# Optimization experiments

Measured on AMD Instinct MI355X. Metric: run time of the kernel, lower is better.

The kernel has to match this reference:

```python
import jax, jax.numpy as jnp
import numpy as np

D = 1024
H = 16
HD = D // H
T = 2048
B = 2
EPS = 1e-6


def rmsnorm(x, w):
    xf = x.astype(jnp.float32)
    n = xf * jax.lax.rsqrt(jnp.mean(xf * xf, axis=-1, keepdims=True) + EPS)
    return n.astype(x.dtype) * w


def setup_inputs() -> dict:
    key = jax.random.key(0)
    ks = jax.random.split(key, 12)
    s_in = 1.0 / np.sqrt(D)
    s_h = 1.0 / np.sqrt(HD * H)
    s_ff = 1.0 / np.sqrt(4 * D)
    return {
        "x": jax.random.normal(ks[0], (B, T, D), jnp.float32),
        "wq": jax.random.normal(ks[1], (H, D, HD), jnp.float32) * s_in,
        "wk": jax.random.normal(ks[2], (H, D, HD), jnp.float32) * s_in,
        "wv": jax.random.normal(ks[3], (H, D, HD), jnp.float32) * s_in,
        "w_proj": jax.random.normal(ks[4], (D, D), jnp.float32) * s_h,
        "b_proj": jax.random.normal(ks[5], (D,), jnp.float32) * 0.01,
        "w1": jax.random.normal(ks[6], (D, 8 * D), jnp.float32) * s_in,
        "b1": jax.random.normal(ks[7], (8 * D,), jnp.float32) * 0.01,
        "w2": jax.random.normal(ks[8], (4 * D, D), jnp.float32) * s_ff,
        "b2": jax.random.normal(ks[9], (D,), jnp.float32) * 0.01,
        "g1": jnp.ones((D,), jnp.float32),
        "g2": jnp.ones((D,), jnp.float32),
    }


def reference(x, wq, wk, wv, w_proj, b_proj, w1, b1, w2, b2, g1, g2):
    # --- attention sub-block ---
    xn = rmsnorm(x, g1)
    q = jnp.einsum("btd,hde->bhte", xn, wq)  # [B,H,T,HD]
    k = jnp.einsum("btd,hde->bhte", xn, wk)
    v = jnp.einsum("btd,hde->bhte", xn, wv)
    scores = jnp.einsum("bhte,bhse->bhts", q, k) * (HD ** -0.5)
    causal = jnp.tril(jnp.ones((T, T), bool))
    scores = jnp.where(causal, scores, -jnp.inf)
    attn = jax.nn.softmax(scores, axis=-1)
    o = jnp.einsum("bhts,bhse->bhte", attn, v)  # [B,H,T,HD]
    o = o.transpose(0, 2, 1, 3).reshape(B, T, H * HD)  # concat heads
    x = x + o @ w_proj + b_proj
    # --- GLU FFN sub-block ---
    xn2 = rmsnorm(x, g2)
    h = xn2 @ w1 + b1  # [B,T,8D]
    a, b = jnp.split(h, 2, axis=-1)
    glu = a * jax.nn.sigmoid(b)  # [B,T,4D]
    x = x + glu @ w2 + b2
    return x
```

## Files before the change

### kernel.cpp

```cpp
#include <hip/hip_runtime.h>


typedef __attribute__((ext_vector_type(4))) float f32x4;
typedef __attribute__((ext_vector_type(8))) short short8;

typedef __attribute__((address_space(1))) const void gvoid;
typedef __attribute__((address_space(3))) void lvoid;

static __device__ __forceinline__ void gl_lds16(const void* g, void* l) {
  __builtin_amdgcn_global_load_lds((gvoid*)g, (lvoid*)l, 16, 0, 0);
}

static __device__ __forceinline__ unsigned short f2bf(float f) {
  union { float f; unsigned u; } v; v.f = f;
  unsigned r = v.u + 0x7fffu + ((v.u >> 16) & 1u);
  return (unsigned short)(r >> 16);
}
static __device__ __forceinline__ float to_f32(float v) { return v; }
static __device__ __forceinline__ float to_f32(unsigned short v) {
  union { unsigned u; float f; } x; x.u = ((unsigned)v) << 16; return x.f;
}

static __device__ __forceinline__ f32x4 mfma16(short8 a, short8 b, f32x4 c) {
  return __builtin_amdgcn_mfma_f32_16x16x32_bf16(a, b, c, 0, 0, 0);
}

template <typename Tin>
__global__ __launch_bounds__(256) void transpose_cvt(
    const Tin* __restrict__ in, unsigned short* __restrict__ out,
    int in_ld, long in_bstride, int out_ld, long out_bstride)
{
  __shared__ float tile[64][65];
  const Tin* inp = in + (long)blockIdx.z * in_bstride;
  unsigned short* outp = out + (long)blockIdx.z * out_bstride;
  int r0 = blockIdx.y * 64, c0 = blockIdx.x * 64;
  int tx = threadIdx.x & 63, ty = threadIdx.x >> 6;
#pragma unroll
  for (int i = ty; i < 64; i += 4)
    tile[i][tx] = to_f32(inp[(long)(r0 + i) * in_ld + (c0 + tx)]);
  __syncthreads();
#pragma unroll
  for (int i = ty; i < 64; i += 4)
    outp[(long)(c0 + i) * out_ld + (r0 + tx)] = f2bf(tile[tx][i]);
}

__global__ __launch_bounds__(256) void qkvw_repack(
    const float* __restrict__ wq, const float* __restrict__ wk,
    const float* __restrict__ wv, unsigned short* __restrict__ out)
{
  __shared__ float tile[64][65];
  const int z = blockIdx.z, head = z & 15, src = z >> 4;
  const float* inp = (src == 0 ? wq : src == 1 ? wk : wv) + (long)head * 1024 * 64;
  unsigned short* outp = out + ((long)src * 1024 + head * 64) * 1024;
  int r0 = blockIdx.y * 64;
  int tx = threadIdx.x & 63, ty = threadIdx.x >> 6;
#pragma unroll
  for (int i = ty; i < 64; i += 4)
    tile[i][tx] = inp[(long)(r0 + i) * 64 + tx];
  __syncthreads();
#pragma unroll
  for (int i = ty; i < 64; i += 4)
    outp[(long)i * 1024 + r0 + tx] = f2bf(tile[tx][i]);
}

__global__ __launch_bounds__(256) void rmsnorm_k(
    const float* __restrict__ x, const float* __restrict__ g,
    unsigned short* __restrict__ out)
{
  int row = blockIdx.x;
  int t = threadIdx.x;
  float4 v = ((const float4*)(x + (long)row * 1024))[t];
  float ss = v.x * v.x + v.y * v.y + v.z * v.z + v.w * v.w;
#pragma unroll
  for (int ofs = 32; ofs; ofs >>= 1) ss += __shfl_down(ss, ofs);
  __shared__ float red[4];
  if ((t & 63) == 0) red[t >> 6] = ss;
  __syncthreads();
  float sc = rsqrtf((red[0] + red[1] + red[2] + red[3]) * (1.0f / 1024.0f) + 1e-6f);
  float4 gv = ((const float4*)g)[t];
  ushort4 o4;
  o4.x = f2bf(v.x * sc * gv.x); o4.y = f2bf(v.y * sc * gv.y);
  o4.z = f2bf(v.z * sc * gv.z); o4.w = f2bf(v.w * sc * gv.w);
  ((ushort4*)(out + (long)row * 1024))[t] = o4;
}

template <int EPI, int BM, int WM_, int WN_, bool GLUB>
__global__ __launch_bounds__(256, 2) void gemm_bt(
    const unsigned short* __restrict__ A, const unsigned short* __restrict__ Bt,
    unsigned short* __restrict__ outb, float* __restrict__ outf,
    const float* __restrict__ res, const float* __restrict__ bias,
    int K, int lda, int ldbt, int ldout)
{
  constexpr int FM = BM / (16 * WM_);
  constexpr int FN = 128 / (16 * WN_);
  constexpr int AR = BM / 32;
  __shared__ alignas(16) unsigned short Asm_[BM * 64];
  __shared__ alignas(16) unsigned short Bsm_[128 * 64];
  const int tid = threadIdx.x, lane = tid & 63, wave = tid >> 6;
  const int lr = lane & 15, lg = lane >> 4;
  const int wr = wave / WN_, wc = wave % WN_;
  const int m0 = blockIdx.y * BM;

  f32x4 acc[FM][FN];
#pragma unroll
  for (int mi = 0; mi < FM; mi++)
#pragma unroll
    for (int ni = 0; ni < FN; ni++) acc[mi][ni] = f32x4{0.f, 0.f, 0.f, 0.f};

  int rr_[4], ru_[4];
  long brow[4];
#pragma unroll
  for (int i = 0; i < 4; i++) {
    int U = tid + 256 * i;
    rr_[i] = U >> 3;
    ru_[i] = ((U & 7) ^ (rr_[i] & 7)) * 8;
    if (GLUB)
      brow[i] = (rr_[i] < 64) ? (long)(blockIdx.x * 64 + rr_[i])
                              : (long)(4096 + blockIdx.x * 64 + rr_[i] - 64);
    else
      brow[i] = (long)blockIdx.x * 128 + rr_[i];
  }

  for (int k0 = 0; k0 < K; k0 += 64) {
#pragma unroll
    for (int i = 0; i < 4; i++) {
      if (i < AR)
        gl_lds16(A + (long)(m0 + rr_[i]) * lda + k0 + ru_[i],
                 (char*)Asm_ + (wave * 64 + 256 * i) * 16);
      gl_lds16(Bt + brow[i] * ldbt + k0 + ru_[i],
               (char*)Bsm_ + (wave * 64 + 256 * i) * 16);
    }
    __syncthreads();

    short8 af[FM][2], bfr[FN][2];
#pragma unroll
    for (int mi = 0; mi < FM; mi++) {
      int row = wr * 16 * FM + mi * 16 + lr;
#pragma unroll
      for (int kk = 0; kk < 2; kk++) {
        int off = row * 128 + (((kk * 4 + lg) ^ (row & 7)) & 7) * 16;
        af[mi][kk] = *(const short8*)((const char*)Asm_ + off);
      }
    }
#pragma unroll
    for (int ni = 0; ni < FN; ni++) {
      int row = wc * 16 * FN + ni * 16 + lr;
#pragma unroll
      for (int kk = 0; kk < 2; kk++) {
        int off = row * 128 + (((kk * 4 + lg) ^ (row & 7)) & 7) * 16;
        bfr[ni][kk] = *(const short8*)((const char*)Bsm_ + off);
      }
    }
#pragma unroll
    for (int kk = 0; kk < 2; kk++)
#pragma unroll
      for (int mi = 0; mi < FM; mi++)
#pragma unroll
        for (int ni = 0; ni < FN; ni++)
          acc[mi][ni] = mfma16(af[mi][kk], bfr[ni][kk], acc[mi][ni]);
    __syncthreads();
  }

  const int rb = m0 + wr * 16 * FM + 4 * lg;
  if constexpr (EPI == 0) {
#pragma unroll
    for (int mi = 0; mi < FM; mi++)
#pragma unroll
      for (int ni = 0; ni < FN; ni++) {
        int col = blockIdx.x * 128 + wc * 16 * FN + ni * 16 + lr;
#pragma unroll
        for (int r = 0; r < 4; r++)
          outb[(long)(rb + mi * 16 + r) * ldout + col] = f2bf(acc[mi][ni][r]);
      }
  } else if constexpr (EPI == 1) {
#pragma unroll
    for (int mi = 0; mi < FM; mi++)
#pragma unroll
      for (int ni = 0; ni < FN; ni++) {
        int col = blockIdx.x * 128 + wc * 16 * FN + ni * 16 + lr;
        float bv = bias[col];
#pragma unroll
        for (int r = 0; r < 4; r++) {
          long idx = (long)(rb + mi * 16 + r) * ldout + col;
          outf[idx] = acc[mi][ni][r] + res[idx] + bv;
        }
      }
  } else {
#pragma unroll
    for (int mi = 0; mi < FM; mi++)
#pragma unroll
      for (int ni = 0; ni < FN / 2; ni++) {
        int col = blockIdx.x * 64 + ni * 16 + lr;
        float ba = bias[col], bb2 = bias[4096 + col];
#pragma unroll
        for (int r = 0; r < 4; r++) {
          float a = acc[mi][ni][r] + ba;
          float b = acc[mi][ni + FN / 2][r] + bb2;
          float s = 1.0f / (1.0f + __expf(-b));
          outb[(long)(rb + mi * 16 + r) * ldout + col] = f2bf(a * s);
        }
      }
  }
}

__global__ __launch_bounds__(256, 2) void attn_k(
    const unsigned short* __restrict__ qkv, const unsigned short* __restrict__ vt,
    unsigned short* __restrict__ o)
{
  __shared__ alignas(16) unsigned short Ksm[2 * 128 * 64];
  __shared__ alignas(16) unsigned short Vsm[2 * 64 * 128];
  __shared__ alignas(16) unsigned short Psm[4][16 * 128];
  const int tid = threadIdx.x, lane = tid & 63, wave = tid >> 6;
  const int lr = lane & 15, lg = lane >> 4;
  const int bh = blockIdx.y, b = bh >> 4, h = bh & 15;
  const int ia = blockIdx.x;
  const int tA0 = ia * 64, tB0 = (31 - ia) * 64;
  const int nchA = (ia + 2) >> 1, nchB = (33 - ia) >> 1;
  const float NEGINF = -__builtin_inff();

  short8 qfA[2], qfB[2];
  {
    const unsigned short* qp =
        qkv + (long)(b * 2048 + tA0 + wave * 16 + lr) * 3072 + h * 64 + lg * 8;
    qfA[0] = *(const short8*)qp;  qfA[1] = *(const short8*)(qp + 32);
    qp = qkv + (long)(b * 2048 + tB0 + wave * 16 + lr) * 3072 + h * 64 + lg * 8;
    qfB[0] = *(const short8*)qp;  qfB[1] = *(const short8*)(qp + 32);
  }
  f32x4 oA[4], oB[4];
#pragma unroll
  for (int n = 0; n < 4; n++) { oA[n] = f32x4{0,0,0,0}; oB[n] = f32x4{0,0,0,0}; }
  float mA = NEGINF, lA = 0.f, mB = NEGINF, lB = 0.f;

  const long kbase = (long)(b * 2048) * 3072 + 1024 + h * 64;
  const long vbase = (long)bh * 64 * 2048;

  auto stage = [&](int buf, int c) {
    const int s0 = c * 128;
#pragma unroll
    for (int i = 0; i < 4; i++) {
      int U = tid + 256 * i;
      int kr = U >> 3, ku = (U ^ kr) & 7;
      gl_lds16(qkv + kbase + (long)(s0 + kr) * 3072 + ku * 8,
               (char*)Ksm + (buf * 1024 + wave * 64 + 256 * i) * 16);
      int vr = U >> 4, vu = (U & 8) | ((U ^ vr) & 7);
      gl_lds16(vt + vbase + (long)vr * 2048 + s0 + vu * 8,
               (char*)Vsm + (buf * 1024 + wave * 64 + 256 * i) * 16);
    }
  };

  char* pb = (char*)&Psm[wave][0];

  auto process = [&](const short8* qf, f32x4* o_acc, float& m, float& l,
                     const char* kb, const char* vb, int s0, int qg, bool diag) {
    f32x4 s[8];
#pragma unroll
    for (int n = 0; n < 8; n++) s[n] = f32x4{0.f, 0.f, 0.f, 0.f};
    __builtin_amdgcn_s_setprio(1);
#pragma unroll
    for (int n = 0; n < 8; n++) {
      int row = n * 16 + lr;
#pragma unroll
      for (int kk = 0; kk < 2; kk++) {
        int off = row * 128 + (((kk * 4 + lg) ^ row) & 7) * 16;
        short8 kf = *(const short8*)(kb + off);
        s[n] = mfma16(kf, qf[kk], s[n]);
      }
    }
    __builtin_amdgcn_s_setprio(0);
#pragma unroll
    for (int n = 0; n < 8; n++)
#pragma unroll
      for (int r = 0; r < 4; r++) {
        float v = s[n][r] * 0.125f;
        if (diag && (s0 + n * 16 + 4 * lg + r > qg)) v = NEGINF;
        s[n][r] = v;
      }
    float t[8];
#pragma unroll
    for (int n = 0; n < 8; n++)
      t[n] = fmaxf(fmaxf(s[n][0], s[n][1]), fmaxf(s[n][2], s[n][3]));
    float mx = fmaxf(fmaxf(fmaxf(t[0], t[1]), fmaxf(t[2], t[3])),
                     fmaxf(fmaxf(t[4], t[5]), fmaxf(t[6], t[7])));
    mx = fmaxf(mx, __shfl_xor(mx, 16));
    mx = fmaxf(mx, __shfl_xor(mx, 32));
    if (!__all(mx <= m + 8.0f)) {
      float mn = fmaxf(m, mx);
      float alpha = __expf(m - mn);
      m = mn;
      l *= alpha;
#pragma unroll
      for (int r = 0; r < 4; r++) {
        float ar = __shfl(alpha, 4 * lg + r);
#pragma unroll
        for (int n = 0; n < 4; n++) o_acc[n][r] *= ar;
      }
    }
    float sum = 0.f;
#pragma unroll
    for (int n = 0; n < 8; n++)
#pragma unroll
      for (int r = 0; r < 4; r++) {
        float p = __expf(s[n][r] - m);
        s[n][r] = p;
        sum += p;
      }
    sum += __shfl_xor(sum, 16);
    sum += __shfl_xor(sum, 32);
    l += sum;
#pragma unroll
    for (int n = 0; n < 8; n++) {
      unsigned lo = (unsigned)f2bf(s[n][0]) | ((unsigned)f2bf(s[n][1]) << 16);
      unsigned hi = (unsigned)f2bf(s[n][2]) | ((unsigned)f2bf(s[n][3]) << 16);
      int u = 2 * n + (lg >> 1);
      int su = (u & 8) | ((u ^ lr) & 7);
      *(uint2*)(pb + lr * 256 + su * 16 + 8 * (lg & 1)) = uint2{lo, hi};
    }
    asm volatile("s_waitcnt lgkmcnt(0)" ::: "memory");
    __builtin_amdgcn_sched_barrier(0);
    short8 pa[4];
#pragma unroll
    for (int ks = 0; ks < 4; ks++) {
      int u = 4 * ks + lg;
      int su = (u & 8) | ((u ^ lr) & 7);
      pa[ks] = *(const short8*)(pb + lr * 256 + su * 16);
    }
    __builtin_amdgcn_s_setprio(1);
#pragma unroll
    for (int n = 0; n < 4; n++) {
      int row = n * 16 + lr;
#pragma unroll
      for (int ks = 0; ks < 4; ks++) {
        int u = 4 * ks + lg;
        int su = (u & 8) | ((u ^ row) & 7);
        short8 vf = *(const short8*)(vb + row * 256 + su * 16);
        o_acc[n] = mfma16(pa[ks], vf, o_acc[n]);
      }
    }
    __builtin_amdgcn_s_setprio(0);
  };

  stage(0, 0);
  __syncthreads();

  const int qgA = tA0 + wave * 16 + lr, qgB = tB0 + wave * 16 + lr;
  for (int c = 0; c < nchB; c++) {
    if (c + 1 < nchB) stage((c + 1) & 1, c + 1);
    const char* kb = (const char*)Ksm + (c & 1) * 16384;
    const char* vb = (const char*)Vsm + (c & 1) * 16384;
    const int s0 = c * 128;
    if (c < nchA) process(qfA, oA, mA, lA, kb, vb, s0, qgA, c == nchA - 1);
    process(qfB, oB, mB, lB, kb, vb, s0, qgB, c == nchB - 1);
    __syncthreads();
  }

  auto finish = [&](const f32x4* o_acc, float l, int t0) {
#pragma unroll
    for (int r = 0; r < 4; r++) {
      float inv = 1.0f / __shfl(l, 4 * lg + r);
      int trow = t0 + wave * 16 + 4 * lg + r;
#pragma unroll
      for (int n = 0; n < 4; n++)
        o[(long)(b * 2048 + trow) * 1024 + h * 64 + n * 16 + lr] =
            f2bf(o_acc[n][r] * inv);
    }
  };
  finish(oA, lA, tA0);
  finish(oB, lB, tB0);
}

extern "C" void kernel_launch(void* const* d_in, const int* in_sizes, int n_in,
                              void* d_out, int out_size, void* d_ws, size_t ws_size,
                              hipStream_t stream) {
  const float* x     = (const float*)d_in[0];
  const float* wq    = (const float*)d_in[1];
  const float* wk    = (const float*)d_in[2];
  const float* wv    = (const float*)d_in[3];
  const float* wproj = (const float*)d_in[4];
  const float* bproj = (const float*)d_in[5];
  const float* w1    = (const float*)d_in[6];
  const float* b1    = (const float*)d_in[7];
  const float* w2    = (const float*)d_in[8];
  const float* b2    = (const float*)d_in[9];
  const float* g1    = (const float*)d_in[10];
  const float* g2    = (const float*)d_in[11];
  (void)in_sizes; (void)n_in; (void)out_size; (void)ws_size;

  char* ws = (char*)d_ws;
  unsigned short* wt_qkv = (unsigned short*)(ws);
  unsigned short* wpt    = (unsigned short*)(ws + (6ul << 20));
  unsigned short* w1t    = (unsigned short*)(ws + (8ul << 20));
  unsigned short* w2t    = (unsigned short*)(ws + (24ul << 20));
  unsigned short* xn     = (unsigned short*)(ws + (32ul << 20));
  unsigned short* qkv    = (unsigned short*)(ws + (40ul << 20));
  unsigned short* vt     = (unsigned short*)(ws + (64ul << 20));
  unsigned short* glu    = (unsigned short*)(ws + (40ul << 20));
  unsigned short* obuf   = (unsigned short*)(ws + (72ul << 20));
  float*          x1     = (float*)(ws + (80ul << 20));
  float* outf = (float*)d_out;

  qkvw_repack<<<dim3(1, 16, 48), 256, 0, stream>>>(wq, wk, wv, wt_qkv);
  transpose_cvt<float><<<dim3(16, 16, 1), 256, 0, stream>>>(
      wproj, wpt, 1024, 0, 1024, 0);
  transpose_cvt<float><<<dim3(128, 16, 1), 256, 0, stream>>>(
      w1, w1t, 8192, 0, 1024, 0);
  transpose_cvt<float><<<dim3(16, 64, 1), 256, 0, stream>>>(
      w2, w2t, 1024, 0, 4096, 0);

  rmsnorm_k<<<4096, 256, 0, stream>>>(x, g1, xn);

  gemm_bt<0, 128, 2, 2, false><<<dim3(24, 32), 256, 0, stream>>>(
      xn, wt_qkv, qkv, nullptr, nullptr, nullptr, 1024, 1024, 1024, 3072);

  transpose_cvt<unsigned short><<<dim3(1, 32, 16), 256, 0, stream>>>(
      qkv + 2048, vt, 3072, 64, 2048, (long)64 * 2048);
  transpose_cvt<unsigned short><<<dim3(1, 32, 16), 256, 0, stream>>>(
      qkv + 2048ul * 3072 + 2048, vt + 16ul * 64 * 2048, 3072, 64, 2048, (long)64 * 2048);

  attn_k<<<dim3(16, 32), 256, 0, stream>>>(qkv, vt, obuf);

  gemm_bt<1, 64, 2, 2, false><<<dim3(8, 64), 256, 0, stream>>>(
      obuf, wpt, nullptr, x1, x, bproj, 1024, 1024, 1024, 1024);

  rmsnorm_k<<<4096, 256, 0, stream>>>(x1, g2, xn);

  gemm_bt<2, 128, 4, 1, true><<<dim3(64, 32), 256, 0, stream>>>(
      xn, w1t, glu, nullptr, nullptr, b1, 1024, 1024, 1024, 4096);

  gemm_bt<1, 64, 2, 2, false><<<dim3(8, 64), 256, 0, stream>>>(
      glu, w2t, nullptr, outf, x1, b2, 4096, 4096, 4096, 1024);
}
```

Baseline: 293.5 us.

## Add 8-wave 256x256-tile GLU GEMM with interleaved load/MFMA pipeline

Replaces the FFN up-projection GEMM with a new 512-thread kernel that computes 256x256 output tiles, with the a and b halves of the GLU interleaved in the B tile so each block emits 128 GLU columns. It double-buffers LDS with direct global-to-LDS loads and interleaves staged loads between MFMA quadrants, separated by barriers and raised wave priority. The goal is more reuse per tile and better overlap of memory with matrix cores. The cost is heavier register and LDS use (64 KB per block), which may limit occupancy.

```diff
diff --git a/kernel.cpp b/kernel.cpp
--- a/kernel.cpp
+++ b/kernel.cpp
@@ -24,6 +24,8 @@
 static __device__ __forceinline__ f32x4 mfma16(short8 a, short8 b, f32x4 c) {
   return __builtin_amdgcn_mfma_f32_16x16x32_bf16(a, b, c, 0, 0, 0);
 }
+
+#define SBAR() asm volatile("s_barrier" ::: "memory")
 
 template <typename Tin>
 __global__ __launch_bounds__(256) void transpose_cvt(
@@ -203,6 +205,164 @@
   }
 }
 
+#define MFMA_Q(AFR, BFR, MI0, NI0)                                          \
+  do {                                                                      \
+    __builtin_amdgcn_s_setprio(1);                                          \
+    _Pragma("unroll") for (int kk_ = 0; kk_ < 2; kk_++)                     \
+    _Pragma("unroll") for (int mi_ = 0; mi_ < 4; mi_++)                     \
+    _Pragma("unroll") for (int ni_ = 0; ni_ < 2; ni_++)                     \
+      acc[(MI0) + mi_][(NI0) + ni_] =                                       \
+          mfma16(AFR[mi_][kk_], BFR[ni_][kk_], acc[(MI0) + mi_][(NI0) + ni_]); \
+    __builtin_amdgcn_s_setprio(0);                                          \
+  } while (0)
+
+__global__ __launch_bounds__(512, 2) void gemm8_glu(
+    const unsigned short* __restrict__ A, const unsigned short* __restrict__ Bt,
+    unsigned short* __restrict__ outb, const float* __restrict__ bias,
+    int K, int lda, int ldbt, int ldout)
+{
+  __shared__ alignas(16) unsigned short Asm_[2][256 * 64];
+  __shared__ alignas(16) unsigned short Bsm_[2][256 * 64];
+  const int tid = threadIdx.x, lane = tid & 63, wave = tid >> 6;
+  const int lr = lane & 15, lg = lane >> 4;
+  const int wr = wave >> 2, wc = wave & 3;
+  const int m0 = blockIdx.y * 256;
+  const int bx = blockIdx.x;
+
+  f32x4 acc[8][4];
+#pragma unroll
+  for (int mi = 0; mi < 8; mi++)
+#pragma unroll
+    for (int ni = 0; ni < 4; ni++) acc[mi][ni] = f32x4{0.f, 0.f, 0.f, 0.f};
+
+  auto stageA = [&](int buf, int h, int k0) {
+#pragma unroll
+    for (int i = 0; i < 2; i++) {
+      int U = tid + 512 * i;
+      int r = U >> 3, s = ((U & 7) ^ (r & 7));
+      gl_lds16(A + (long)(m0 + h * 128 + r) * lda + k0 + s * 8,
+               (char*)&Asm_[buf][0] + h * 16384 + U * 16);
+    }
+  };
+  auto stageB = [&](int buf, int h, int k0) {
+#pragma unroll
+    for (int i = 0; i < 2; i++) {
+      int U = tid + 512 * i;
+      int r = U >> 3, s = ((U & 7) ^ (r & 7));
+      int row = h * 128 + r;
+      int g = row >> 5;
+      long brow = (long)((g & 1) ? 4096 : 0) + bx * 128 + (g >> 1) * 32 + (row & 31);
+      gl_lds16(Bt + brow * ldbt + k0 + s * 8,
+               (char*)&Bsm_[buf][0] + h * 16384 + U * 16);
+    }
+  };
+  auto lda8 = [&](int buf, int mi, int kk) -> short8 {
+    int row = wr * 128 + mi * 16 + lr;
+    return *(const short8*)((const char*)&Asm_[buf][0] + row * 128 +
+                            (((kk * 4 + lg) ^ (row & 7)) * 16));
+  };
+  auto ldb8 = [&](int buf, int ni, int kk) -> short8 {
+    int row = wc * 64 + ni * 16 + lr;
+    return *(const short8*)((const char*)&Bsm_[buf][0] + row * 128 +
+                            (((kk * 4 + lg) ^ (row & 7)) * 16));
+  };
+
+  stageA(0, 0, 0); stageA(0, 1, 0); stageB(0, 0, 0); stageB(0, 1, 0);
+  stageA(1, 0, 64);
+  asm volatile("s_waitcnt vmcnt(2)" ::: "memory");
+  SBAR();
+
+  short8 af[4][2], bf0[2][2], bf1[2][2];
+  const int NIT = K / 128;
+  for (int it = 0; it < NIT; ++it) {
+    const int k0 = it * 128;
+    const bool last = (it == NIT - 1);
+#pragma unroll
+    for (int mi = 0; mi < 4; mi++)
+#pragma unroll
+      for (int kk = 0; kk < 2; kk++) af[mi][kk] = lda8(0, mi, kk);
+#pragma unroll
+    for (int ni = 0; ni < 2; ni++)
+#pragma unroll
+      for (int kk = 0; kk < 2; kk++) bf0[ni][kk] = ldb8(0, ni, kk);
+    stageA(1, 1, k0 + 64);
+    SBAR();
+    MFMA_Q(af, bf0, 0, 0);
+    SBAR();
+#pragma unroll
+    for (int ni = 0; ni < 2; ni++)
+#pragma unroll
+      for (int kk = 0; kk < 2; kk++) bf1[ni][kk] = ldb8(0, ni + 2, kk);
+    stageB(1, 0, k0 + 64);
+    SBAR();
+    MFMA_Q(af, bf1, 0, 2);
+    SBAR();
+#pragma unroll
+    for (int mi = 0; mi < 4; mi++)
+#pragma unroll
+      for (int kk = 0; kk < 2; kk++) af[mi][kk] = lda8(0, mi + 4, kk);
+    stageB(1, 1, k0 + 64);
+    SBAR();
+    MFMA_Q(af, bf1, 4, 2);
+    SBAR();
+    if (!last) stageA(0, 0, k0 + 128);
+    SBAR();
+    MFMA_Q(af, bf0, 4, 0);
+    if (last) asm volatile("s_waitcnt vmcnt(0)" ::: "memory");
+    else      asm volatile("s_waitcnt vmcnt(2)" ::: "memory");
+    SBAR();
+#pragma unroll
+    for (int mi = 0; mi < 4; mi++)
+#pragma unroll
+      for (int kk = 0; kk < 2; kk++) af[mi][kk] = lda8(1, mi, kk);
+#pragma unroll
+    for (int ni = 0; ni < 2; ni++)
+#pragma unroll
+      for (int kk = 0; kk < 2; kk++) bf0[ni][kk] = ldb8(1, ni, kk);
+    if (!last) stageA(0, 1, k0 + 128);
+    SBAR();
+    MFMA_Q(af, bf0, 0, 0);
+    SBAR();
+#pragma unroll
+    for (int ni = 0; ni < 2; ni++)
+#pragma unroll
+      for (int kk = 0; kk < 2; kk++) bf1[ni][kk] = ldb8(1, ni + 2, kk);
+    if (!last) stageB(0, 0, k0 + 128);
+    SBAR();
+    MFMA_Q(af, bf1, 0, 2);
+    SBAR();
+#pragma unroll
+    for (int mi = 0; mi < 4; mi++)
+#pragma unroll
+      for (int kk = 0; kk < 2; kk++) af[mi][kk] = lda8(1, mi + 4, kk);
+    if (!last) stageB(0, 1, k0 + 128);
+    SBAR();
+    MFMA_Q(af, bf1, 4, 2);
+    SBAR();
+    if (it + 1 < NIT) stageA(1, 0, k0 + 192);
+    SBAR();
+    MFMA_Q(af, bf0, 4, 0);
+    if (!last) asm volatile("s_waitcnt vmcnt(2)" ::: "memory");
+    SBAR();
+  }
+
+#pragma unroll
+  for (int mi = 0; mi < 8; mi++)
+#pragma unroll
+    for (int ni = 0; ni < 2; ni++) {
+      int col = bx * 128 + wc * 32 + ni * 16 + lr;
+      float ba = bias[col], bb = bias[4096 + col];
+#pragma unroll
+      for (int r = 0; r < 4; r++) {
+        int row = m0 + wr * 128 + mi * 16 + 4 * lg + r;
+        float a = acc[mi][ni][r] + ba;
+        float b = acc[mi][ni + 2][r] + bb;
+        float s = 1.0f / (1.0f + __expf(-b));
+        outb[(long)row * ldout + col] = f2bf(a * s);
+      }
+    }
+}
+
 __global__ __launch_bounds__(256, 2) void attn_k(
     const unsigned short* __restrict__ qkv, const unsigned short* __restrict__ vt,
     unsigned short* __restrict__ o)
@@ -423,8 +583,8 @@
 
   rmsnorm_k<<<4096, 256, 0, stream>>>(x1, g2, xn);
 
-  gemm_bt<2, 128, 4, 1, true><<<dim3(64, 32), 256, 0, stream>>>(
-      xn, w1t, glu, nullptr, nullptr, b1, 1024, 1024, 1024, 4096);
+  gemm8_glu<<<dim3(32, 16), 512, 0, stream>>>(
+      xn, w1t, glu, b1, 1024, 1024, 1024, 4096);
 
   gemm_bt<1, 64, 2, 2, false><<<dim3(8, 64), 256, 0, stream>>>(
       glu, w2t, nullptr, outf, x1, b2, 4096, 4096, 4096, 1024);
```

New measurement: 296.2 us. About the same (+0.9%).
